# Kernel optimization log

Hardware: AMD Instinct MI355X
Metric: run time of the kernel (lower is better)

## Reference

```python
import jax, jax.numpy as jnp
import numpy as np

H = 768
NH = 12
HD = 64
R = 4
SCALING = 8.0 / 4.0  # lora_alpha / r


def setup_inputs() -> dict:
    key = jax.random.key(0)
    ks = jax.random.split(key, 16)
    B, T = 16, 512
    s = 0.02
    x = jax.random.normal(ks[0], (B, T, H), dtype=jnp.float32)
    mask = jax.random.randint(ks[1], (B, T), 0, 2, dtype=jnp.int32)
    return {
        "x": x,
        "mask": mask,
        "Wq": jax.random.normal(ks[2], (H, H), jnp.float32) * s,
        "bq": jnp.zeros((H,), jnp.float32),
        "Aq": jax.random.normal(ks[3], (R, H), jnp.float32) * s,
        "Bq": jax.random.normal(ks[4], (H, R), jnp.float32) * s,
        "Wk": jax.random.normal(ks[5], (H, H), jnp.float32) * s,
        "bk": jnp.zeros((H,), jnp.float32),
        "Wv": jax.random.normal(ks[6], (H, H), jnp.float32) * s,
        "bv": jnp.zeros((H,), jnp.float32),
        "Av": jax.random.normal(ks[7], (R, H), jnp.float32) * s,
        "Bv": jax.random.normal(ks[8], (H, R), jnp.float32) * s,
        "Wo": jax.random.normal(ks[9], (H, H), jnp.float32) * s,
        "bo": jnp.zeros((H,), jnp.float32),
    }


def _lora_linear(x, W, b, A, Bm):
    # base: x @ W^T + b ; lora: (x @ A^T) @ B^T * scaling (dropout inactive at eval)
    return x @ W.T + b + (x @ A.T) @ Bm.T * SCALING


def reference(x, mask, Wq, bq, Aq, Bq, Wk, bk, Wv, bv, Av, Bv, Wo, bo):
    B, T, _ = x.shape
    q = _lora_linear(x, Wq, bq, Aq, Bq).reshape(B, T, NH, HD).transpose(0, 2, 1, 3)
    k = (x @ Wk.T + bk).reshape(B, T, NH, HD).transpose(0, 2, 1, 3)
    v = _lora_linear(x, Wv, bv, Av, Bv).reshape(B, T, NH, HD).transpose(0, 2, 1, 3)
    # [B, NH, T, T]
    scores = jnp.einsum("bhqd,bhkd->bhqk", q, k) / jnp.sqrt(jnp.float32(HD))
    m = (mask == 0)[:, None, None, :]  # mask key positions where mask==0
    scores = jnp.where(m, jnp.float32(-1e9), scores)
    attn = jax.nn.softmax(scores, axis=-1)  # dropout inactive at eval
    out = jnp.einsum("bhqk,bhkd->bhqd", attn, v)
    out = out.transpose(0, 2, 1, 3).reshape(B, T, H)
    return out @ Wo.T + bo
```

## Files before the change

### kernel.cpp

```cpp
#include <hip/hip_runtime.h>
#include <stdint.h>

#define H 768
#define NHEAD 12
#define HDIM 64
#define BATCH 16
#define TSEQ 512
#define BT (BATCH*TSEQ)
#define C3 (3*H)

typedef __attribute__((ext_vector_type(8))) short short8;
typedef __attribute__((ext_vector_type(4))) float floatx4;
typedef unsigned short u16;

__device__ __forceinline__ u16 f2bf(float f) {
    union { float f; unsigned int u; } v; v.f = f;
    unsigned int u = v.u;
    return (u16)((u + 0x7FFFu + ((u >> 16) & 1u)) >> 16);
}

__device__ __forceinline__ void async_ld16(const void* g, void* l) {
    __builtin_amdgcn_global_load_lds((__attribute__((address_space(1))) void*)g,
                                     (__attribute__((address_space(3))) void*)l,
                                     16, 0, 0);
}

#define PREP_BLOCKS 9216
#define CVT_BLOCKS  6144
__global__ void prep_kernel(const float* __restrict__ Wq, const float* __restrict__ bq,
                            const float* __restrict__ Aq, const float* __restrict__ Bq,
                            const float* __restrict__ Wk, const float* __restrict__ bk,
                            const float* __restrict__ Wv, const float* __restrict__ bv,
                            const float* __restrict__ Av, const float* __restrict__ Bv,
                            const float* __restrict__ Wo, const float* __restrict__ x,
                            u16* __restrict__ Wall, u16* __restrict__ Wobf,
                            float* __restrict__ bias_all, u16* __restrict__ xb)
{
    const int bid = blockIdx.x;
    if (bid >= PREP_BLOCKS) {
        const int i = ((bid - PREP_BLOCKS) * 256 + threadIdx.x) * 4;
        const float4 v = *(const float4*)(x + i);
        u16 o[4] = { f2bf(v.x), f2bf(v.y), f2bf(v.z), f2bf(v.w) };
        *(uint2*)(xb + i) = *(const uint2*)o;
        return;
    }
    const int idx = bid * 256 + threadIdx.x;
    const int r = idx / H;
    const int c = idx - r * H;
    if (r < H) {
        float v = Wq[idx] + 2.0f * (Bq[r*4+0]*Aq[c] + Bq[r*4+1]*Aq[H+c] +
                                    Bq[r*4+2]*Aq[2*H+c] + Bq[r*4+3]*Aq[3*H+c]);
        Wall[idx] = f2bf(v);
    } else if (r < 2*H) {
        Wall[idx] = f2bf(Wk[idx - H*H]);
    } else if (r < 3*H) {
        const int rr = r - 2*H;
        float v = Wv[rr*H + c] + 2.0f * (Bv[rr*4+0]*Av[c] + Bv[rr*4+1]*Av[H+c] +
                                         Bv[rr*4+2]*Av[2*H+c] + Bv[rr*4+3]*Av[3*H+c]);
        Wall[idx] = f2bf(v);
    } else {
        Wobf[idx - 3*H*H] = f2bf(Wo[idx - 3*H*H]);
    }
    if (idx < C3) {
        bias_all[idx] = (idx < H) ? bq[idx] : (idx < 2*H ? bk[idx - H] : bv[idx - 2*H]);
    }
}

template<int MODE, int TM, int NN>
__global__ __launch_bounds__(256)
void gemm_bt(const u16* __restrict__ A, const u16* __restrict__ Bw,
             const float* __restrict__ bias, void* __restrict__ Cout,
             int K, int ldc)
{
    constexpr int MT = TM / 32;
    __shared__ u16 Ablk[TM * 64];
    __shared__ u16 Bblk[128 * 64];
    const int tid  = threadIdx.x;
    const int wave = tid >> 6;
    const int lane = tid & 63;
    const int quad = lane >> 4;
    const int l16  = lane & 15;

    const int j   = blockIdx.x;
    const int nM  = gridDim.x / NN;
    const int Mx  = nM >> 3;
    const int xcd = j & 7;
    const int loc = j >> 3;
    const int dm  = loc & (Mx - 1);
    const int nb  = loc / Mx;
    const int m0 = (xcd + 8*dm) * TM;
    const int n0 = nb * 128;

    const int mw = (wave & 1) * (TM / 2);
    const int nw = (wave >> 1) * 64;

    const int r8 = lane >> 3;
    const int kgs = ((lane & 7) ^ r8) * 8;
    const u16* gA = A  + (size_t)(m0 + wave*(TM/4) + r8) * K + kgs;
    const u16* gB = Bw + (size_t)(n0 + wave*32      + r8) * K + kgs;
    u16* lA = Ablk + wave * (TM/4) * 64;
    u16* lB = Bblk + wave * 32 * 64;

    floatx4 acc[MT][4] = {};
    const int sw = l16 & 7;

    for (int k0 = 0; k0 < K; k0 += 64) {
        __syncthreads();
        #pragma unroll
        for (int jj = 0; jj < TM/32; jj++)
            async_ld16(gA + k0 + (size_t)(jj*8) * K, lA + jj*8*64);
        #pragma unroll
        for (int jj = 0; jj < 4; jj++)
            async_ld16(gB + k0 + (size_t)(jj*8) * K, lB + jj*8*64);
        __syncthreads();
        #pragma unroll
        for (int kk = 0; kk < 2; kk++) {
            short8 af[MT], bfr[4];
            #pragma unroll
            for (int mt = 0; mt < MT; mt++)
                af[mt] = *(const short8*)(Ablk + (mw + mt*16 + l16)*64 + ((quad + 4*kk) ^ sw)*8);
            #pragma unroll
            for (int nt = 0; nt < 4; nt++)
                bfr[nt] = *(const short8*)(Bblk + (nw + nt*16 + l16)*64 + ((quad + 4*kk) ^ sw)*8);
            #pragma unroll
            for (int mt = 0; mt < MT; mt++)
                #pragma unroll
                for (int nt = 0; nt < 4; nt++)
                    acc[mt][nt] = __builtin_amdgcn_mfma_f32_16x16x32_bf16(af[mt], bfr[nt], acc[mt][nt], 0, 0, 0);
        }
    }

    #pragma unroll
    for (int nt = 0; nt < 4; nt++) {
        const int n = n0 + nw + nt*16 + l16;
        const float bv = bias[n];
        #pragma unroll
        for (int mt = 0; mt < MT; mt++) {
            #pragma unroll
            for (int r = 0; r < 4; r++) {
                const int m = m0 + mw + mt*16 + quad*4 + r;
                const float v = acc[mt][nt][r] + bv;
                if (MODE == 1) ((u16*)Cout)[(size_t)m * ldc + n] = f2bf(v);
                else           ((float*)Cout)[(size_t)m * ldc + n] = v;
            }
        }
    }
}

#define TSTRIDE 72
__global__ __launch_bounds__(256)
void vtrans_kernel(const u16* __restrict__ qkv, u16* __restrict__ vt)
{
    __shared__ u16 Lt[64 * TSTRIDE];
    const int tc = blockIdx.x;
    const int bh = blockIdx.y;
    const int b = bh / NHEAD, h = bh - b * NHEAD;
    const int tid = threadIdx.x;

    {
        const int tok = tid & 63;
        const int dg  = (tid >> 6) * 16;
        const u16* p = qkv + (size_t)(b*TSEQ + tc*64 + tok) * C3 + 2*H + h*HDIM + dg;
        u16 tmp[16];
        *(short8*)tmp       = *(const short8*)p;
        *(short8*)(tmp + 8) = *(const short8*)(p + 8);
        #pragma unroll
        for (int j = 0; j < 16; j++) Lt[(dg + j) * TSTRIDE + tok] = tmp[j];
    }
    __syncthreads();
    {
        const int d  = tid >> 2;
        const int ts = (tid & 3) * 16;
        uint4 a0 = *(const uint4*)(Lt + d * TSTRIDE + ts);
        uint4 a1 = *(const uint4*)(Lt + d * TSTRIDE + ts + 8);
        u16* op = vt + ((size_t)bh * HDIM + d) * TSEQ + tc*64 + ts;
        *(uint4*)op       = a0;
        *(uint4*)(op + 8) = a1;
    }
}

#define PSTRIDE 40

__global__ __launch_bounds__(256)
void attn_kernel(const u16* __restrict__ qkv, const u16* __restrict__ vt,
                 const int* __restrict__ mask, u16* __restrict__ attn_out)
{
    __shared__ float maskadd[TSEQ];
    __shared__ u16 Kbuf[2][32 * 64];
    __shared__ u16 Vbuf[2][64 * 32];
    __shared__ u16 Pbuf[4][2][16 * PSTRIDE];

    const int qt = blockIdx.x;
    const int bh = blockIdx.y;
    const int b = bh / NHEAD, h = bh - b * NHEAD;
    const int tid  = threadIdx.x;
    const int wave = tid >> 6;
    const int lane = tid & 63;
    const int quad = lane >> 4;
    const int l16  = lane & 15;

    for (int i = tid; i < TSEQ; i += 256)
        maskadd[i] = (mask[b*TSEQ + i] == 0) ? -1e9f : 0.0f;

    const size_t btok = (size_t)b * TSEQ;
    const int q0 = qt * 128 + wave * 32;

    short8 qf[2][2];
    #pragma unroll
    for (int m = 0; m < 2; m++) {
        const u16* qp = qkv + (btok + q0 + m*16 + l16) * C3 + h*HDIM + quad*8;
        qf[m][0] = *(const short8*)qp;
        qf[m][1] = *(const short8*)(qp + 32);
    }

    const u16* kglob = qkv + btok * C3 + H + h*HDIM;
    const u16* vglob = vt + (size_t)bh * HDIM * TSEQ;

    auto stage = [&](int kb, int pp) {
        {
            const int r = lane >> 3;
            const int g = (lane & 7) ^ r;
            async_ld16(kglob + (size_t)(kb + wave*8 + r) * C3 + g*8,
                       &Kbuf[pp][wave*8*64]);
        }
        {
            const int dr = lane >> 2;
            const int g  = (lane & 3) ^ ((dr >> 1) & 3);
            async_ld16(vglob + (size_t)(wave*16 + dr) * TSEQ + kb + g*8,
                       &Vbuf[pp][wave*16*32]);
        }
    };

    floatx4 o[2][4] = {};
    float lsum[2][4] = {};

    auto compute = [&](int kb, int pp) {
        const u16* Kb_ = Kbuf[pp];
        const u16* Vb_ = Vbuf[pp];
        short8 kf[2][2];
        #pragma unroll
        for (int t = 0; t < 2; t++)
            #pragma unroll
            for (int h2 = 0; h2 < 2; h2++)
                kf[t][h2] = *(const short8*)(Kb_ + (t*16 + l16)*64 + (((h2*4 + quad) ^ (l16 & 7))*8));
        short8 vf[4];
        #pragma unroll
        for (int dt = 0; dt < 4; dt++)
            vf[dt] = *(const short8*)(Vb_ + (dt*16 + l16)*32 + ((quad ^ ((l16 >> 1) & 3))*8));

        floatx4 s[2][2];
        #pragma unroll
        for (int m = 0; m < 2; m++)
            #pragma unroll
            for (int t = 0; t < 2; t++) {
                floatx4 acc = {0.f, 0.f, 0.f, 0.f};
                acc = __builtin_amdgcn_mfma_f32_16x16x32_bf16(qf[m][0], kf[t][0], acc, 0, 0, 0);
                acc = __builtin_amdgcn_mfma_f32_16x16x32_bf16(qf[m][1], kf[t][1], acc, 0, 0, 0);
                s[m][t] = acc;
            }
        const float m0 = maskadd[kb + l16];
        const float m1 = maskadd[kb + 16 + l16];
        #pragma unroll
        for (int m = 0; m < 2; m++) {
            u16* Pw = Pbuf[wave][m];
            #pragma unroll
            for (int r = 0; r < 4; r++) {
                const float p0 = __expf(s[m][0][r] * 0.125f + m0);
                const float p1 = __expf(s[m][1][r] * 0.125f + m1);
                lsum[m][r] += p0 + p1;
                Pw[(quad*4 + r) * PSTRIDE + l16]      = f2bf(p0);
                Pw[(quad*4 + r) * PSTRIDE + 16 + l16] = f2bf(p1);
            }
        }
        #pragma unroll
        for (int m = 0; m < 2; m++) {
            const short8 pa = *(const short8*)(Pbuf[wave][m] + l16 * PSTRIDE + quad*8);
            #pragma unroll
            for (int dt = 0; dt < 4; dt++)
                o[m][dt] = __builtin_amdgcn_mfma_f32_16x16x32_bf16(pa, vf[dt], o[m][dt], 0, 0, 0);
        }
    };

    stage(0, 0);
    for (int it = 0; it < 16; it++) {
        __syncthreads();
        if (it < 15) stage((it + 1) * 32, (it + 1) & 1);
        compute(it * 32, it & 1);
    }

    #pragma unroll
    for (int m = 0; m < 2; m++) {
        float inv[4];
        #pragma unroll
        for (int r = 0; r < 4; r++) {
            float l = lsum[m][r];
            l += __shfl_xor(l, 1);
            l += __shfl_xor(l, 2);
            l += __shfl_xor(l, 4);
            l += __shfl_xor(l, 8);
            inv[r] = 1.0f / l;
        }
        #pragma unroll
        for (int dt = 0; dt < 4; dt++)
            #pragma unroll
            for (int r = 0; r < 4; r++) {
                const int q = q0 + m*16 + quad*4 + r;
                attn_out[(btok + q) * H + h*HDIM + dt*16 + l16] = f2bf(o[m][dt][r] * inv[r]);
            }
    }
}

extern "C" void kernel_launch(void* const* d_in, const int* in_sizes, int n_in,
                              void* d_out, int out_size, void* d_ws, size_t ws_size,
                              hipStream_t stream)
{
    const float* x   = (const float*)d_in[0];
    const int* mask  = (const int*)d_in[1];
    const float* Wq  = (const float*)d_in[2];
    const float* bq  = (const float*)d_in[3];
    const float* Aq  = (const float*)d_in[4];
    const float* Bq  = (const float*)d_in[5];
    const float* Wk  = (const float*)d_in[6];
    const float* bk  = (const float*)d_in[7];
    const float* Wv  = (const float*)d_in[8];
    const float* bv  = (const float*)d_in[9];
    const float* Av  = (const float*)d_in[10];
    const float* Bv  = (const float*)d_in[11];
    const float* Wo  = (const float*)d_in[12];
    const float* bo  = (const float*)d_in[13];

    char* ws = (char*)d_ws;
    u16*   xb      = (u16*)  (ws);
    u16*   Wall    = (u16*)  (ws + 12582912);
    u16*   Wobf    = (u16*)  (ws + 16121856);
    float* biasall = (float*)(ws + 17301504);
    u16*   qkv     = (u16*)  (ws + 17310720);
    u16*   attn_o  = (u16*)  (ws + 55059456);
    u16*   vt      = xb;

    prep_kernel<<<PREP_BLOCKS + CVT_BLOCKS, 256, 0, stream>>>(
        Wq, bq, Aq, Bq, Wk, bk, Wv, bv, Av, Bv, Wo, x, Wall, Wobf, biasall, xb);
    gemm_bt<1,128,18><<<18 * (BT/128), 256, 0, stream>>>(xb, Wall, biasall, qkv, H, C3);
    vtrans_kernel<<<dim3(TSEQ/64, BATCH*NHEAD), 256, 0, stream>>>(qkv, vt);
    attn_kernel<<<dim3(TSEQ/128, BATCH*NHEAD), 256, 0, stream>>>(qkv, vt, mask, attn_o);
    gemm_bt<0,64,6><<<6 * (BT/64), 256, 0, stream>>>(attn_o, Wobf, bo, d_out, H, H);
}
```

Baseline: 212.9 us.

## Compute V transposed directly via swapped-operand GEMM, dropping vtrans kernel

Splits the fused QKV projection into a Q/K GEMM with a 1536-wide output and a separate V GEMM. The V GEMM swaps operands (weights as A, activations as B) and writes its result straight into the per-head transposed [b,h,d,t] layout, so the separate V transpose kernel and its round trip through memory go away. The cost is an extra GEMM launch, and the transposed-store epilogue writes scattered 2-byte elements, though 16 lanes do write consecutive t values. V output now gets its own workspace region instead of reusing the xb buffer.

Result: faster. 201.5 us (-5.4%).

```diff
diff --git a/kernel.cpp b/kernel.cpp
--- a/kernel.cpp
+++ b/kernel.cpp
@@ -8,6 +8,7 @@
 #define TSEQ 512
 #define BT (BATCH*TSEQ)
 #define C3 (3*H)
+#define LDQK 1536
 
 typedef __attribute__((ext_vector_type(8))) short short8;
 typedef __attribute__((ext_vector_type(4))) float floatx4;
@@ -66,7 +67,7 @@
     }
 }
 
-template<int MODE, int TM, int NN>
+template<int MODE, int TM, int NB, int MB, int MAP>
 __global__ __launch_bounds__(256)
 void gemm_bt(const u16* __restrict__ A, const u16* __restrict__ Bw,
              const float* __restrict__ bias, void* __restrict__ Cout,
@@ -81,15 +82,24 @@
     const int quad = lane >> 4;
     const int l16  = lane & 15;
 
-    const int j   = blockIdx.x;
-    const int nM  = gridDim.x / NN;
-    const int Mx  = nM >> 3;
-    const int xcd = j & 7;
-    const int loc = j >> 3;
-    const int dm  = loc & (Mx - 1);
-    const int nb  = loc / Mx;
-    const int m0 = (xcd + 8*dm) * TM;
-    const int n0 = nb * 128;
+    int m0, n0;
+    {
+        const int j   = blockIdx.x;
+        const int xcd = j & 7;
+        const int loc = j >> 3;
+        if (MAP == 0) {
+            constexpr int Mx = MB / 8;
+            const int dm = loc % Mx;
+            const int nb = loc / Mx;
+            m0 = (xcd + 8*dm) * TM;
+            n0 = nb * 128;
+        } else {
+            const int dm = loc % MB;
+            const int nl = loc / MB;
+            m0 = dm * TM;
+            n0 = (xcd + 8*nl) * 128;
+        }
+    }
 
     const int mw = (wave & 1) * (TM / 2);
     const int nw = (wave >> 1) * 64;
@@ -130,59 +140,46 @@
         }
     }
 
-    #pragma unroll
-    for (int nt = 0; nt < 4; nt++) {
-        const int n = n0 + nw + nt*16 + l16;
-        const float bv = bias[n];
+    if (MODE == 2) {
         #pragma unroll
         for (int mt = 0; mt < MT; mt++) {
             #pragma unroll
             for (int r = 0; r < 4; r++) {
-                const int m = m0 + mw + mt*16 + quad*4 + r;
-                const float v = acc[mt][nt][r] + bv;
-                if (MODE == 1) ((u16*)Cout)[(size_t)m * ldc + n] = f2bf(v);
-                else           ((float*)Cout)[(size_t)m * ldc + n] = v;
-            }
-        }
-    }
-}
-
-#define TSTRIDE 72
+                const int m  = m0 + mw + mt*16 + quad*4 + r;
+                const float bv = bias[m];
+                const int hh = m >> 6, d = m & 63;
+                #pragma unroll
+                for (int nt = 0; nt < 4; nt++) {
+                    const int n = n0 + nw + nt*16 + l16;
+                    const int b = n >> 9, t = n & 511;
+                    ((u16*)Cout)[((size_t)((b*NHEAD + hh)*HDIM + d))*TSEQ + t]
+                        = f2bf(acc[mt][nt][r] + bv);
+                }
+            }
+        }
+    } else {
+        #pragma unroll
+        for (int nt = 0; nt < 4; nt++) {
+            const int n = n0 + nw + nt*16 + l16;
+            const float bv = bias[n];
+            #pragma unroll
+            for (int mt = 0; mt < MT; mt++) {
+                #pragma unroll
+                for (int r = 0; r < 4; r++) {
+                    const int m = m0 + mw + mt*16 + quad*4 + r;
+                    const float v = acc[mt][nt][r] + bv;
+                    if (MODE == 1) ((u16*)Cout)[(size_t)m * ldc + n] = f2bf(v);
+                    else           ((float*)Cout)[(size_t)m * ldc + n] = v;
+                }
+            }
+        }
+    }
+}
+
+#define PSTRIDE 40
+
 __global__ __launch_bounds__(256)
-void vtrans_kernel(const u16* __restrict__ qkv, u16* __restrict__ vt)
-{
-    __shared__ u16 Lt[64 * TSTRIDE];
-    const int tc = blockIdx.x;
-    const int bh = blockIdx.y;
-    const int b = bh / NHEAD, h = bh - b * NHEAD;
-    const int tid = threadIdx.x;
-
-    {
-        const int tok = tid & 63;
-        const int dg  = (tid >> 6) * 16;
-        const u16* p = qkv + (size_t)(b*TSEQ + tc*64 + tok) * C3 + 2*H + h*HDIM + dg;
-        u16 tmp[16];
-        *(short8*)tmp       = *(const short8*)p;
-        *(short8*)(tmp + 8) = *(const short8*)(p + 8);
-        #pragma unroll
-        for (int j = 0; j < 16; j++) Lt[(dg + j) * TSTRIDE + tok] = tmp[j];
-    }
-    __syncthreads();
-    {
-        const int d  = tid >> 2;
-        const int ts = (tid & 3) * 16;
-        uint4 a0 = *(const uint4*)(Lt + d * TSTRIDE + ts);
-        uint4 a1 = *(const uint4*)(Lt + d * TSTRIDE + ts + 8);
-        u16* op = vt + ((size_t)bh * HDIM + d) * TSEQ + tc*64 + ts;
-        *(uint4*)op       = a0;
-        *(uint4*)(op + 8) = a1;
-    }
-}
-
-#define PSTRIDE 40
-
-__global__ __launch_bounds__(256)
-void attn_kernel(const u16* __restrict__ qkv, const u16* __restrict__ vt,
+void attn_kernel(const u16* __restrict__ qk, const u16* __restrict__ vt,
                  const int* __restrict__ mask, u16* __restrict__ attn_out)
 {
     __shared__ float maskadd[TSEQ];
@@ -208,19 +205,19 @@
     short8 qf[2][2];
     #pragma unroll
     for (int m = 0; m < 2; m++) {
-        const u16* qp = qkv + (btok + q0 + m*16 + l16) * C3 + h*HDIM + quad*8;
+        const u16* qp = qk + (btok + q0 + m*16 + l16) * LDQK + h*HDIM + quad*8;
         qf[m][0] = *(const short8*)qp;
         qf[m][1] = *(const short8*)(qp + 32);
     }
 
-    const u16* kglob = qkv + btok * C3 + H + h*HDIM;
+    const u16* kglob = qk + btok * LDQK + H + h*HDIM;
     const u16* vglob = vt + (size_t)bh * HDIM * TSEQ;
 
     auto stage = [&](int kb, int pp) {
         {
             const int r = lane >> 3;
             const int g = (lane & 7) ^ r;
-            async_ld16(kglob + (size_t)(kb + wave*8 + r) * C3 + g*8,
+            async_ld16(kglob + (size_t)(kb + wave*8 + r) * LDQK + g*8,
                        &Kbuf[pp][wave*8*64]);
         }
         {
@@ -334,14 +331,15 @@
     u16*   Wall    = (u16*)  (ws + 12582912);
     u16*   Wobf    = (u16*)  (ws + 16121856);
     float* biasall = (float*)(ws + 17301504);
-    u16*   qkv     = (u16*)  (ws + 17310720);
+    u16*   qk      = (u16*)  (ws + 17310720);
+    u16*   vt      = (u16*)  (ws + 42476544);
     u16*   attn_o  = (u16*)  (ws + 55059456);
-    u16*   vt      = xb;
 
     prep_kernel<<<PREP_BLOCKS + CVT_BLOCKS, 256, 0, stream>>>(
         Wq, bq, Aq, Bq, Wk, bk, Wv, bv, Av, Bv, Wo, x, Wall, Wobf, biasall, xb);
-    gemm_bt<1,128,18><<<18 * (BT/128), 256, 0, stream>>>(xb, Wall, biasall, qkv, H, C3);
-    vtrans_kernel<<<dim3(TSEQ/64, BATCH*NHEAD), 256, 0, stream>>>(qkv, vt);
-    attn_kernel<<<dim3(TSEQ/128, BATCH*NHEAD), 256, 0, stream>>>(qkv, vt, mask, attn_o);
-    gemm_bt<0,64,6><<<6 * (BT/64), 256, 0, stream>>>(attn_o, Wobf, bo, d_out, H, H);
-}
+    gemm_bt<1,128,12,64,0><<<12*64, 256, 0, stream>>>(xb, Wall, biasall, qk, H, LDQK);
+    gemm_bt<2,64,64,12,1><<<64*12, 256, 0, stream>>>(Wall + (size_t)2*H*H, xb,
+                                                     biasall + 2*H, vt, H, 0);
+    attn_kernel<<<dim3(TSEQ/128, BATCH*NHEAD), 256, 0, stream>>>(qk, vt, mask, attn_o);
+    gemm_bt<0,64,6,128,0><<<6*128, 256, 0, stream>>>(attn_o, Wobf, bo, d_out, H, H);
+}
```
